# Kernel optimization log

Hardware: AMD Instinct MI355X
Metric: run time of the kernel (lower is better)

The kernel has to match this reference:

```python
import jax, jax.numpy as jnp
import numpy as np

BETA = 0.999      # EMA momentum from __init__ default
MIN_PTS = 256     # per-class minimum point count from forward()
EPS = 1e-12       # torch F.normalize eps


def _l2norm(v):
    n = jnp.sqrt(jnp.sum(v * v, axis=1, keepdims=True))
    return v / jnp.maximum(n, EPS)


def setup_inputs() -> dict:
    key = jax.random.key(0)
    ks = jax.random.split(key, 14)
    B, N, CIN = 4, 40000, 4
    ENC_H, ENC_D, PROJ_H, PRIOR_D, NC = 256, 512, 256, 128, 13
    s = 0.02
    pos = jax.random.normal(ks[0], (B, N, 3), jnp.float32)
    x = jax.random.normal(ks[1], (B, CIN, N), jnp.float32)
    y = jax.random.randint(ks[2], (B, N), 0, NC)
    # pointwise encoder stand-in (real encoder is an opaque external PointNeXt)
    W_enc1 = jax.random.normal(ks[3], (CIN + 3, ENC_H), jnp.float32) * s
    b_enc1 = jnp.zeros((ENC_H,), jnp.float32)
    W_enc2 = jax.random.normal(ks[4], (ENC_H, ENC_D), jnp.float32) * s
    b_enc2 = jnp.zeros((ENC_D,), jnp.float32)
    # projection head: Linear(512->256) ReLU Linear(256->128) ReLU
    W1 = jax.random.normal(ks[5], (ENC_D, PROJ_H), jnp.float32) * s
    b1 = jnp.zeros((PROJ_H,), jnp.float32)
    W2 = jax.random.normal(ks[6], (PROJ_H, PRIOR_D), jnp.float32) * s
    b2 = jnp.zeros((PRIOR_D,), jnp.float32)
    prior_ema = _l2norm(jax.random.uniform(ks[7], (NC, PRIOR_D), jnp.float32))
    return {"pos": pos, "x": x, "y": y,
            "W_enc1": W_enc1, "b_enc1": b_enc1, "W_enc2": W_enc2, "b_enc2": b_enc2,
            "W1": W1, "b1": b1, "W2": W2, "b2": b2, "prior_ema": prior_ema}


def reference(pos, x, y, W_enc1, b_enc1, W_enc2, b_enc2, W1, b1, W2, b2, prior_ema):
    NC = prior_ema.shape[0]
    p0 = pos.reshape(-1, pos.shape[-1])                       # [P, 3]
    f0 = jnp.transpose(x, (0, 2, 1)).reshape(-1, x.shape[1])  # [P, C]
    labels = y.reshape(-1)                                    # [P]
    # per-class counts and the >=256 validity gate (replaces the Python class loop)
    counts = jax.ops.segment_sum(jnp.ones(labels.shape, jnp.float32), labels, num_segments=NC)
    valid = counts >= MIN_PTS                                 # [NC]
    # encoder stand-in: pointwise MLP on (features, coords)
    h = jax.nn.relu(jnp.concatenate([f0, p0], axis=1) @ W_enc1 + b_enc1)
    enc = jax.nn.relu(h @ W_enc2 + b_enc2)                    # [P, 512]
    # projection head + L2 normalize
    g = jax.nn.relu(enc @ W1 + b1)
    feat = jax.nn.relu(g @ W2 + b2)                           # [P, 128]
    feat = _l2norm(feat)
    # current_prior: features + float label column (-1 marks dropped classes)
    lbl_eff = jnp.where(valid[labels], labels, -1)
    current_prior = jnp.concatenate([feat, lbl_eff[:, None].astype(feat.dtype)], axis=1)
    # _ema: detached per-class segment mean, keep old prior for empty/invalid classes
    fsg = jax.lax.stop_gradient(feat)
    sums = jax.ops.segment_sum(fsg, labels, num_segments=NC)  # [NC, 128]
    means = sums / jnp.maximum(counts, 1.0)[:, None]
    cur = jnp.where(valid[:, None], means, prior_ema)
    new_prior = _l2norm(BETA * prior_ema + (1.0 - BETA) * cur)
    return current_prior, new_prior
```

## Files before the change

kernel.cpp:

```cpp
#include <hip/hip_runtime.h>
#include <hip/hip_bf16.h>

#define P_TOTAL 160000
#define NPB     40000
#define NCLS    13
#define TP      64
#define NBLK    (P_TOTAL / TP)

typedef __attribute__((ext_vector_type(8))) short bf16x8;
typedef __attribute__((ext_vector_type(4))) float f32x4;

__device__ __forceinline__ ushort f2bf(float f) {
  union { float f; unsigned u; } v; v.f = f;
  return (ushort)((v.u + 0x8000) >> 16);
}

__device__ __forceinline__ void transpose_tile(const float* __restrict__ src,
                                               ushort* __restrict__ dst,
                                               int K, int N, int tile, ushort (*t)[33]) {
  int ntx = N >> 5;
  int n0 = (tile % ntx) << 5, k0 = (tile / ntx) << 5;
  int c = threadIdx.x & 31, r = threadIdx.x >> 5;
  #pragma unroll
  for (int rr = 0; rr < 32; rr += 8)
    t[r + rr][c] = f2bf(src[(k0 + r + rr) * N + n0 + c]);
  __syncthreads();
  #pragma unroll
  for (int rr = 0; rr < 32; rr += 8)
    dst[(n0 + r + rr) * K + k0 + c] = t[c][r + rr];
}

__global__ void prep_all_kernel(const float* __restrict__ We1, const float* __restrict__ We2,
                                const float* __restrict__ W1,  const float* __restrict__ W2,
                                const int* __restrict__ y,
                                ushort* __restrict__ WT1, ushort* __restrict__ WT2,
                                ushort* __restrict__ WT3, ushort* __restrict__ WT4,
                                int* __restrict__ counts) {
  __shared__ ushort t[32][33];
  __shared__ int h[NCLS];
  int b = blockIdx.x, tid = threadIdx.x;
  if (b < 128)       transpose_tile(We2, WT2, 256, 512, b, t);
  else if (b < 256)  transpose_tile(W1,  WT3, 512, 256, b - 128, t);
  else if (b < 288)  transpose_tile(W2,  WT4, 256, 128, b - 256, t);
  else if (b == 288) {
    for (int i = tid; i < 8192; i += 256) {
      int n = i >> 5, k = i & 31;
      WT1[i] = (k < 7) ? f2bf(We1[k * 256 + n]) : (ushort)0;
    }
  } else {
    if (tid < NCLS) h[tid] = 0;
    __syncthreads();
    for (int i = (b - 289) * 256 + tid; i < P_TOTAL; i += 127 * 256)
      atomicAdd(&h[y[i]], 1);
    __syncthreads();
    if (tid < NCLS) atomicAdd(&counts[tid], h[tid]);
  }
}

__global__ __launch_bounds__(512, 4) void main_kernel(
    const float* __restrict__ pos, const float* __restrict__ x, const int* __restrict__ y,
    const float* __restrict__ be1, const float* __restrict__ be2,
    const float* __restrict__ b1,  const float* __restrict__ b2,
    const ushort* __restrict__ WT1, const ushort* __restrict__ WT2,
    const ushort* __restrict__ WT3, const ushort* __restrict__ WT4,
    const int* __restrict__ counts, float* __restrict__ gsums, int* __restrict__ done,
    const float* __restrict__ prior, float* __restrict__ out) {
  __shared__ ushort actbuf[TP * 264];
  __shared__ ushort chunkbuf[TP * 136];
  __shared__ float  inv_norm[TP];
  __shared__ float  lbl_eff[TP];
  __shared__ int    lbl[TP];
  __shared__ float  invn[NCLS];
  __shared__ int    is_last;

  const int tid  = threadIdx.x;
  const int wave = tid >> 6, lane = tid & 63;
  const int quad = lane >> 4, mrow = lane & 15;
  const long p0 = (long)blockIdx.x * TP;
  const int bb = (int)(p0 / NPB);
  const int n0 = (int)(p0 % NPB);
  const f32x4 zero = {0.f, 0.f, 0.f, 0.f};

  for (int i = tid; i < TP * 40; i += 512) {
    int r = i / 40, k = i - r * 40;
    float v = 0.f;
    if (k < 4)      v = x[(bb * 4 + k) * NPB + n0 + r];
    else if (k < 7) v = pos[(p0 + r) * 3 + (k - 4)];
    chunkbuf[r * 40 + k] = f2bf(v);
  }
  if (tid < TP) lbl[tid] = y[p0 + tid];
  __syncthreads();

  {
    f32x4 acc1[4][2];
    #pragma unroll
    for (int mt = 0; mt < 4; mt++) { acc1[mt][0] = zero; acc1[mt][1] = zero; }
    const int kl = quad << 3;
    bf16x8 af[4], bw[2];
    #pragma unroll
    for (int mt = 0; mt < 4; mt++)
      af[mt] = *(const bf16x8*)(&chunkbuf[0] + (mt * 16 + mrow) * 40 + kl);
    #pragma unroll
    for (int nt = 0; nt < 2; nt++)
      bw[nt] = *(const bf16x8*)(WT1 + (wave * 32 + nt * 16 + mrow) * 32 + kl);
    #pragma unroll
    for (int nt = 0; nt < 2; nt++)
      #pragma unroll
      for (int mt = 0; mt < 4; mt++)
        acc1[mt][nt] = __builtin_amdgcn_mfma_f32_16x16x32_bf16(af[mt], bw[nt], acc1[mt][nt], 0, 0, 0);
    #pragma unroll
    for (int nt = 0; nt < 2; nt++) {
      int n = wave * 32 + nt * 16 + mrow;
      float bv = be1[n];
      #pragma unroll
      for (int mt = 0; mt < 4; mt++)
        #pragma unroll
        for (int r = 0; r < 4; r++)
          actbuf[(mt * 16 + quad * 4 + r) * 264 + n] = f2bf(fmaxf(acc1[mt][nt][r] + bv, 0.f));
    }
  }
  __syncthreads();

  f32x4 acc3[4][2];
  #pragma unroll
  for (int mt = 0; mt < 4; mt++) { acc3[mt][0] = zero; acc3[mt][1] = zero; }

  ushort* const cb = &chunkbuf[0];
  for (int c = 0; c < 4; c++) {
    f32x4 acc2[4];
    #pragma unroll
    for (int mt = 0; mt < 4; mt++) acc2[mt] = zero;
    #pragma unroll
    for (int ks = 0; ks < 8; ks++) {
      const int kl = ks * 32 + (quad << 3);
      bf16x8 af[4];
      #pragma unroll
      for (int mt = 0; mt < 4; mt++)
        af[mt] = *(const bf16x8*)(actbuf + (mt * 16 + mrow) * 264 + kl);
      bf16x8 bw = *(const bf16x8*)(WT2 + (long)(c * 128 + wave * 16 + mrow) * 256 + kl);
      #pragma unroll
      for (int mt = 0; mt < 4; mt++)
        acc2[mt] = __builtin_amdgcn_mfma_f32_16x16x32_bf16(af[mt], bw, acc2[mt], 0, 0, 0);
    }
    if (c) __syncthreads();
    {
      int lc = wave * 16 + mrow;
      float bv = be2[c * 128 + lc];
      #pragma unroll
      for (int mt = 0; mt < 4; mt++)
        #pragma unroll
        for (int r = 0; r < 4; r++)
          cb[(mt * 16 + quad * 4 + r) * 136 + lc] = f2bf(fmaxf(acc2[mt][r] + bv, 0.f));
    }
    __syncthreads();
    #pragma unroll
    for (int ks = 0; ks < 4; ks++) {
      const int kl = ks * 32 + (quad << 3);
      bf16x8 af[4], bw[2];
      #pragma unroll
      for (int mt = 0; mt < 4; mt++)
        af[mt] = *(const bf16x8*)(cb + (mt * 16 + mrow) * 136 + kl);
      #pragma unroll
      for (int nt = 0; nt < 2; nt++)
        bw[nt] = *(const bf16x8*)(WT3 + (long)(wave * 32 + nt * 16 + mrow) * 512 + c * 128 + kl);
      #pragma unroll
      for (int nt = 0; nt < 2; nt++)
        #pragma unroll
        for (int mt = 0; mt < 4; mt++)
          acc3[mt][nt] = __builtin_amdgcn_mfma_f32_16x16x32_bf16(af[mt], bw[nt], acc3[mt][nt], 0, 0, 0);
    }
  }

  #pragma unroll
  for (int nt = 0; nt < 2; nt++) {
    int n = wave * 32 + nt * 16 + mrow;
    float bv = b1[n];
    #pragma unroll
    for (int mt = 0; mt < 4; mt++)
      #pragma unroll
      for (int r = 0; r < 4; r++)
        actbuf[(mt * 16 + quad * 4 + r) * 264 + n] = f2bf(fmaxf(acc3[mt][nt][r] + bv, 0.f));
  }
  __syncthreads();

  float* const part = (float*)&chunkbuf[0];

  f32x4 acc4[4];
  #pragma unroll
  for (int mt = 0; mt < 4; mt++) acc4[mt] = zero;
  #pragma unroll
  for (int ks = 0; ks < 8; ks++) {
    const int kl = ks * 32 + (quad << 3);
    bf16x8 af[4];
    #pragma unroll
    for (int mt = 0; mt < 4; mt++)
      af[mt] = *(const bf16x8*)(actbuf + (mt * 16 + mrow) * 264 + kl);
    bf16x8 bw = *(const bf16x8*)(WT4 + (long)(wave * 16 + mrow) * 256 + kl);
    #pragma unroll
    for (int mt = 0; mt < 4; mt++)
      acc4[mt] = __builtin_amdgcn_mfma_f32_16x16x32_bf16(af[mt], bw, acc4[mt], 0, 0, 0);
  }
  const int col = wave * 16 + mrow;
  float val[4][4];
  {
    float bv = b2[col];
    #pragma unroll
    for (int mt = 0; mt < 4; mt++)
      #pragma unroll
      for (int r = 0; r < 4; r++)
        val[mt][r] = fmaxf(acc4[mt][r] + bv, 0.f);
  }

  #pragma unroll
  for (int mt = 0; mt < 4; mt++)
    #pragma unroll
    for (int r = 0; r < 4; r++) {
      float s = val[mt][r] * val[mt][r];
      s += __shfl_xor(s, 1);  s += __shfl_xor(s, 2);
      s += __shfl_xor(s, 4);  s += __shfl_xor(s, 8);
      if (mrow == 0) part[wave * TP + mt * 16 + quad * 4 + r] = s;
    }
  __syncthreads();
  if (tid < TP) {
    float ss = 0.f;
    #pragma unroll
    for (int w = 0; w < 8; w++) ss += part[w * TP + tid];
    inv_norm[tid] = 1.f / fmaxf(sqrtf(ss), 1e-12f);
    int l = lbl[tid];
    lbl_eff[tid] = (counts[l] >= 256) ? (float)l : -1.f;
  }
  __syncthreads();

  float a[NCLS];
  #pragma unroll
  for (int cc = 0; cc < NCLS; cc++) a[cc] = 0.f;
  #pragma unroll
  for (int mt = 0; mt < 4; mt++)
    #pragma unroll
    for (int r = 0; r < 4; r++) {
      int R = mt * 16 + quad * 4 + r;
      float vn = val[mt][r] * inv_norm[R];
      out[(p0 + R) * 129 + col] = vn;
      int cls = lbl[R];
      #pragma unroll
      for (int cc = 0; cc < NCLS; cc++) a[cc] += (cls == cc) ? vn : 0.f;
    }
  if (tid < TP) out[(p0 + tid) * 129 + 128] = lbl_eff[tid];
  #pragma unroll
  for (int cc = 0; cc < NCLS; cc++) {
    a[cc] += __shfl_xor(a[cc], 16);
    a[cc] += __shfl_xor(a[cc], 32);
  }
  if (quad == 0)
    #pragma unroll
    for (int cc = 0; cc < NCLS; cc++) atomicAdd(&gsums[cc * 128 + col], a[cc]);

  __syncthreads();
  if (tid == 0) {
    int old = atomicAdd(done, 1);
    is_last = (old == NBLK - 1);
  }
  __syncthreads();
  if (!is_last) return;

  float* vbuf = (float*)actbuf;
  for (int i = tid; i < NCLS * 128; i += 512) {
    float g = atomicAdd(&gsums[i], 0.f);
    int cls = i >> 7;
    int cnt = counts[cls];
    float mean = g / fmaxf((float)cnt, 1.f);
    float pr = prior[i];
    float cur = (cnt >= 256) ? mean : pr;
    vbuf[i] = 0.999f * pr + 0.001f * cur;
  }
  __syncthreads();
  if (tid < NCLS) {
    float s = 0.f;
    for (int c = 0; c < 128; c++) { float t = vbuf[tid * 128 + c]; s += t * t; }
    invn[tid] = 1.f / fmaxf(sqrtf(s), 1e-12f);
  }
  __syncthreads();
  for (int i = tid; i < NCLS * 128; i += 512)
    out[(long)P_TOTAL * 129 + i] = vbuf[i] * invn[i >> 7];
}

extern "C" void kernel_launch(void* const* d_in, const int* in_sizes, int n_in,
                              void* d_out, int out_size, void* d_ws, size_t ws_size,
                              hipStream_t stream) {
  const float* pos   = (const float*)d_in[0];
  const float* x     = (const float*)d_in[1];
  const int*   y     = (const int*)  d_in[2];
  const float* We1   = (const float*)d_in[3];
  const float* be1   = (const float*)d_in[4];
  const float* We2   = (const float*)d_in[5];
  const float* be2   = (const float*)d_in[6];
  const float* W1    = (const float*)d_in[7];
  const float* b1    = (const float*)d_in[8];
  const float* W2    = (const float*)d_in[9];
  const float* b2    = (const float*)d_in[10];
  const float* prior = (const float*)d_in[11];
  float* out = (float*)d_out;

  char* ws = (char*)d_ws;
  int*    counts = (int*)   (ws + 0);
  float*  gsums  = (float*) (ws + 256);
  int*    done   = (int*)   (ws + 7168);
  ushort* WT1    = (ushort*)(ws + 8192);
  ushort* WT2    = (ushort*)(ws + 24576);
  ushort* WT3    = (ushort*)(ws + 286720);
  ushort* WT4    = (ushort*)(ws + 548864);

  hipMemsetAsync(ws, 0, 8192, stream);
  prep_all_kernel<<<416, 256, 0, stream>>>(We1, We2, W1, W2, y, WT1, WT2, WT3, WT4, counts);
  main_kernel    <<<NBLK, 512, 0, stream>>>(pos, x, y, be1, be2, b1, b2,
                                            WT1, WT2, WT3, WT4, counts, gsums, done, prior, out);
}
```

Before: 344.2 us.

## Use 2x2 wave tiling for layers 2 and 4, reduce class sums via LDS atomics

Layers 2 and 4 switch from each wave covering all 64 rows times 16 columns to a 2x2 tile per wave (32 rows times 32 columns). This cuts the A-fragment LDS loads per MFMA from one per MFMA to half. The per-class feature sums change from 13 register accumulators with shuffle reduction plus global atomics from every wave to shared-memory atomics into an LDS csum array. That array is then flushed to global with one atomic per element. The new scheme adds LDS atomic contention and a barrier, and it issues global atomics for all 1664 entries even when a class is absent from the block.

```diff
diff --git a/kernel.cpp b/kernel.cpp
--- a/kernel.cpp
+++ b/kernel.cpp
@@ -125,32 +125,37 @@
   #pragma unroll
   for (int mt = 0; mt < 4; mt++) { acc3[mt][0] = zero; acc3[mt][1] = zero; }
 
+  const int wr2 = wave >> 2, wc2 = wave & 3;
   ushort* const cb = &chunkbuf[0];
   for (int c = 0; c < 4; c++) {
-    f32x4 acc2[4];
-    #pragma unroll
-    for (int mt = 0; mt < 4; mt++) acc2[mt] = zero;
+    f32x4 acc2[2][2];
+    acc2[0][0] = zero; acc2[0][1] = zero; acc2[1][0] = zero; acc2[1][1] = zero;
     #pragma unroll
     for (int ks = 0; ks < 8; ks++) {
       const int kl = ks * 32 + (quad << 3);
-      bf16x8 af[4];
-      #pragma unroll
-      for (int mt = 0; mt < 4; mt++)
-        af[mt] = *(const bf16x8*)(actbuf + (mt * 16 + mrow) * 264 + kl);
-      bf16x8 bw = *(const bf16x8*)(WT2 + (long)(c * 128 + wave * 16 + mrow) * 256 + kl);
-      #pragma unroll
-      for (int mt = 0; mt < 4; mt++)
-        acc2[mt] = __builtin_amdgcn_mfma_f32_16x16x32_bf16(af[mt], bw, acc2[mt], 0, 0, 0);
+      bf16x8 af[2], bw[2];
+      #pragma unroll
+      for (int mt = 0; mt < 2; mt++)
+        af[mt] = *(const bf16x8*)(actbuf + (wr2 * 32 + mt * 16 + mrow) * 264 + kl);
+      #pragma unroll
+      for (int nt = 0; nt < 2; nt++)
+        bw[nt] = *(const bf16x8*)(WT2 + (long)(c * 128 + wc2 * 32 + nt * 16 + mrow) * 256 + kl);
+      #pragma unroll
+      for (int nt = 0; nt < 2; nt++)
+        #pragma unroll
+        for (int mt = 0; mt < 2; mt++)
+          acc2[mt][nt] = __builtin_amdgcn_mfma_f32_16x16x32_bf16(af[mt], bw[nt], acc2[mt][nt], 0, 0, 0);
     }
     if (c) __syncthreads();
-    {
-      int lc = wave * 16 + mrow;
+    #pragma unroll
+    for (int nt = 0; nt < 2; nt++) {
+      int lc = wc2 * 32 + nt * 16 + mrow;
       float bv = be2[c * 128 + lc];
       #pragma unroll
-      for (int mt = 0; mt < 4; mt++)
+      for (int mt = 0; mt < 2; mt++)
         #pragma unroll
         for (int r = 0; r < 4; r++)
-          cb[(mt * 16 + quad * 4 + r) * 136 + lc] = f2bf(fmaxf(acc2[mt][r] + bv, 0.f));
+          cb[(wr2 * 32 + mt * 16 + quad * 4 + r) * 136 + lc] = f2bf(fmaxf(acc2[mt][nt][r] + bv, 0.f));
     }
     __syncthreads();
     #pragma unroll
@@ -184,76 +189,80 @@
   __syncthreads();
 
   float* const part = (float*)&chunkbuf[0];
-
-  f32x4 acc4[4];
-  #pragma unroll
-  for (int mt = 0; mt < 4; mt++) acc4[mt] = zero;
+  float* const csum = (float*)&chunkbuf[2048];
+  for (int i = tid; i < NCLS * 128; i += 512) csum[i] = 0.f;
+
+  const int wr4 = wave & 1, wc4 = wave >> 1;
+  f32x4 acc4[2][2];
+  acc4[0][0] = zero; acc4[0][1] = zero; acc4[1][0] = zero; acc4[1][1] = zero;
   #pragma unroll
   for (int ks = 0; ks < 8; ks++) {
     const int kl = ks * 32 + (quad << 3);
-    bf16x8 af[4];
-    #pragma unroll
-    for (int mt = 0; mt < 4; mt++)
-      af[mt] = *(const bf16x8*)(actbuf + (mt * 16 + mrow) * 264 + kl);
-    bf16x8 bw = *(const bf16x8*)(WT4 + (long)(wave * 16 + mrow) * 256 + kl);
-    #pragma unroll
-    for (int mt = 0; mt < 4; mt++)
-      acc4[mt] = __builtin_amdgcn_mfma_f32_16x16x32_bf16(af[mt], bw, acc4[mt], 0, 0, 0);
-  }
-  const int col = wave * 16 + mrow;
-  float val[4][4];
-  {
-    float bv = b2[col];
-    #pragma unroll
-    for (int mt = 0; mt < 4; mt++)
+    bf16x8 af[2], bw[2];
+    #pragma unroll
+    for (int mt = 0; mt < 2; mt++)
+      af[mt] = *(const bf16x8*)(actbuf + (wr4 * 32 + mt * 16 + mrow) * 264 + kl);
+    #pragma unroll
+    for (int nt = 0; nt < 2; nt++)
+      bw[nt] = *(const bf16x8*)(WT4 + (long)(wc4 * 32 + nt * 16 + mrow) * 256 + kl);
+    #pragma unroll
+    for (int nt = 0; nt < 2; nt++)
+      #pragma unroll
+      for (int mt = 0; mt < 2; mt++)
+        acc4[mt][nt] = __builtin_amdgcn_mfma_f32_16x16x32_bf16(af[mt], bw[nt], acc4[mt][nt], 0, 0, 0);
+  }
+  float val[2][2][4];
+  #pragma unroll
+  for (int nt = 0; nt < 2; nt++) {
+    float bv = b2[wc4 * 32 + nt * 16 + mrow];
+    #pragma unroll
+    for (int mt = 0; mt < 2; mt++)
       #pragma unroll
       for (int r = 0; r < 4; r++)
-        val[mt][r] = fmaxf(acc4[mt][r] + bv, 0.f);
-  }
-
-  #pragma unroll
-  for (int mt = 0; mt < 4; mt++)
-    #pragma unroll
-    for (int r = 0; r < 4; r++) {
-      float s = val[mt][r] * val[mt][r];
-      s += __shfl_xor(s, 1);  s += __shfl_xor(s, 2);
-      s += __shfl_xor(s, 4);  s += __shfl_xor(s, 8);
-      if (mrow == 0) part[wave * TP + mt * 16 + quad * 4 + r] = s;
-    }
+        val[mt][nt][r] = fmaxf(acc4[mt][nt][r] + bv, 0.f);
+  }
+
+  #pragma unroll
+  for (int mt = 0; mt < 2; mt++)
+    #pragma unroll
+    for (int nt = 0; nt < 2; nt++)
+      #pragma unroll
+      for (int r = 0; r < 4; r++) {
+        float s = val[mt][nt][r] * val[mt][nt][r];
+        s += __shfl_xor(s, 1);  s += __shfl_xor(s, 2);
+        s += __shfl_xor(s, 4);  s += __shfl_xor(s, 8);
+        if (mrow == 0) part[(wc4 * 2 + nt) * TP + wr4 * 32 + mt * 16 + quad * 4 + r] = s;
+      }
   __syncthreads();
   if (tid < TP) {
     float ss = 0.f;
     #pragma unroll
-    for (int w = 0; w < 8; w++) ss += part[w * TP + tid];
+    for (int g = 0; g < 8; g++) ss += part[g * TP + tid];
     inv_norm[tid] = 1.f / fmaxf(sqrtf(ss), 1e-12f);
     int l = lbl[tid];
     lbl_eff[tid] = (counts[l] >= 256) ? (float)l : -1.f;
   }
   __syncthreads();
 
-  float a[NCLS];
-  #pragma unroll
-  for (int cc = 0; cc < NCLS; cc++) a[cc] = 0.f;
-  #pragma unroll
-  for (int mt = 0; mt < 4; mt++)
+  #pragma unroll
+  for (int mt = 0; mt < 2; mt++)
     #pragma unroll
     for (int r = 0; r < 4; r++) {
-      int R = mt * 16 + quad * 4 + r;
-      float vn = val[mt][r] * inv_norm[R];
-      out[(p0 + R) * 129 + col] = vn;
+      int R = wr4 * 32 + mt * 16 + quad * 4 + r;
+      float in = inv_norm[R];
       int cls = lbl[R];
       #pragma unroll
-      for (int cc = 0; cc < NCLS; cc++) a[cc] += (cls == cc) ? vn : 0.f;
+      for (int nt = 0; nt < 2; nt++) {
+        int cc = wc4 * 32 + nt * 16 + mrow;
+        float vn = val[mt][nt][r] * in;
+        out[(p0 + R) * 129 + cc] = vn;
+        atomicAdd(&csum[cls * 128 + cc], vn);
+      }
     }
   if (tid < TP) out[(p0 + tid) * 129 + 128] = lbl_eff[tid];
-  #pragma unroll
-  for (int cc = 0; cc < NCLS; cc++) {
-    a[cc] += __shfl_xor(a[cc], 16);
-    a[cc] += __shfl_xor(a[cc], 32);
-  }
-  if (quad == 0)
-    #pragma unroll
-    for (int cc = 0; cc < NCLS; cc++) atomicAdd(&gsums[cc * 128 + col], a[cc]);
+  __syncthreads();
+  for (int i = tid; i < NCLS * 128; i += 512)
+    atomicAdd(&gsums[i], csum[i]);
 
   __syncthreads();
   if (tid == 0) {
```

Measured after the change: 501.7 us. 45.7% more time.
